# Kernel tuning notes

Measured on AMD Instinct MI355X. Metric: run time of the kernel, lower is better.

Reference implementation:

```python
import jax, jax.numpy as jnp
import numpy as np

R_MAX = 6.0
P = 6.0
QQ = 14.399645 * 0.5  # metal units, * 0.5


def setup_inputs() -> dict:
    key = jax.random.key(0)
    k1, k2, k3, k4 = jax.random.split(key, 4)
    n_atoms = 100_000
    n_edges = 6_400_000
    num_types = 4
    # atomic numbers for H, C, O, Cu
    Z = jnp.asarray([1.0, 6.0, 8.0, 29.0], dtype=jnp.float32)
    # edge lengths in (0.1, 7.3) so some edges exceed r_max and get cut off
    r = jax.random.uniform(k1, (n_edges,), dtype=jnp.float32) * 7.2 + 0.1
    per_atom_energy = jax.random.normal(k2, (n_atoms, 1), dtype=jnp.float32)
    atom_types = jax.random.randint(k3, (n_atoms,), 0, num_types, dtype=jnp.int64)
    edge_index = jax.random.randint(k4, (2, n_edges), 0, n_atoms, dtype=jnp.int64)
    return {"Z": Z, "r": r, "per_atom_energy": per_atom_energy,
            "atom_types": atom_types, "edge_index": edge_index}


def _zbl_edge_energy(Z, r, atom_types, edge_index):
    pzbl = 0.23
    a0 = 0.4685
    c1, c2, c3, c4 = 0.02817, 0.28022, 0.50986, 0.18175
    d1, d2, d3, d4 = -0.20162, -0.4029, -0.94229, -3.1998
    edge_types = atom_types[edge_index]          # (2, E)
    Zpair = Z[edge_types]                        # (2, E)
    Zi, Zj = Zpair[0], Zpair[1]
    x = (jnp.power(Zi, pzbl) + jnp.power(Zj, pzbl)) * r / a0
    psi = (c1 * jnp.exp(d1 * x) + c2 * jnp.exp(d2 * x)
           + c3 * jnp.exp(d3 * x) + c4 * jnp.exp(d4 * x))
    eng = QQ * (Zi * Zj / r) * psi
    rr = r / R_MAX
    p = P
    cutoff = (1.0 - (p + 1.0) * (p + 2.0) / 2.0 * jnp.power(rr, p)
              + p * (p + 2.0) * jnp.power(rr, p + 1.0)
              - p * (p + 1.0) / 2.0 * jnp.power(rr, p + 2.0))
    cutoff = cutoff * (rr < 1.0).astype(cutoff.dtype)
    return cutoff * eng                          # (E,)


def reference(Z, r, per_atom_energy, atom_types, edge_index):
    edge_eng = _zbl_edge_energy(Z, r, atom_types, edge_index)
    n_atoms = per_atom_energy.shape[0]
    atomic_eng = jax.ops.segment_sum(edge_eng, edge_index[0],
                                     num_segments=n_atoms)[:, None]
    return atomic_eng + per_atom_energy
```

## Files before the change

kernel.cpp:

```cpp
#include <hip/hip_runtime.h>


namespace {
constexpr float PZBL     = 0.23f;
constexpr float A0_INV   = 1.0f / 0.4685f;
constexpr float C1 = 0.02817f, C2 = 0.28022f, C3 = 0.50986f, C4 = 0.18175f;
constexpr float D1 = -0.20162f, D2 = -0.4029f, D3 = -0.94229f, D4 = -3.1998f;
constexpr float QQ       = 14.399645f * 0.5f;
constexpr float RMAX_INV = 1.0f / 6.0f;
constexpr int   CHUNK    = 25600;
constexpr int   BLOCK    = 1024;
constexpr int   S_MAX    = 64;
}

__global__ void zbl_table_kernel(const float* __restrict__ Z,
                                 float* __restrict__ tbl) {
    int t = threadIdx.x;
    if (t < 4) {
        float z = Z[t];
        tbl[t]     = z;
        tbl[4 + t] = powf(z, PZBL);
    }
}

__device__ __forceinline__ float zbl_energy(float rk, int ia, int ib,
                                            const int* __restrict__ types,
                                            const float* s_z, const float* s_zp) {
    float rr = rk * RMAX_INV;
    int ti = types[ia];
    int tj = types[ib];
    float zi = s_z[ti], zj = s_z[tj];
    float x = (s_zp[ti] + s_zp[tj]) * rk * A0_INV;
    float psi = C1 * __expf(D1 * x) + C2 * __expf(D2 * x)
              + C3 * __expf(D3 * x) + C4 * __expf(D4 * x);
    float eng = QQ * zi * zj * psi / rk;
    float rr2 = rr * rr;
    float rr3 = rr2 * rr;
    float rr6 = rr3 * rr3;
    float cutoff = 1.0f + rr6 * (-28.0f + rr * (48.0f - 21.0f * rr));
    return cutoff * eng;
}

__device__ __forceinline__ void zbl_edge_lds(float rk, int ia, int ib, int base,
                                             const int* __restrict__ types,
                                             const float* s_z, const float* s_zp,
                                             float* bins) {
    unsigned d = (unsigned)(ia - base);
    if (d >= (unsigned)CHUNK) return;
    if (rk * RMAX_INV >= 1.0f) return;
    atomicAdd(&bins[d], zbl_energy(rk, ia, ib, types, s_z, s_zp));
}

__global__ __launch_bounds__(BLOCK) void zbl_chunk_kernel(
    const float* __restrict__ r,
    const int*   __restrict__ ei0,
    const int*   __restrict__ ei1,
    const int*   __restrict__ types,
    const float* __restrict__ tbl,
    float*       __restrict__ partials,
    int n_chunks, int n_slices, int quads_per_slice,
    int n_quads, int n_edges) {
    __shared__ float s_z[4];
    __shared__ float s_zp[4];
    __shared__ float bins[CHUNK];

    int tid = threadIdx.x;
    if (tid < 8) {
        if (tid < 4) s_z[tid] = tbl[tid];
        else         s_zp[tid - 4] = tbl[tid];
    }
    for (int i = tid; i < CHUNK; i += BLOCK) bins[i] = 0.0f;
    __syncthreads();

    const int c = blockIdx.x % n_chunks;
    const int s = blockIdx.x / n_chunks;
    const int base = c * CHUNK;

    const int q0 = s * quads_per_slice;
    const int q1 = min(n_quads, q0 + quads_per_slice);
    const float4* r4 = (const float4*)r;
    const int4*   a4 = (const int4*)ei0;
    const int4*   b4 = (const int4*)ei1;

    for (int q = q0 + tid; q < q1; q += BLOCK) {
        float4 rv = r4[q];
        int4   av = a4[q];
        int4   bv = b4[q];
        zbl_edge_lds(rv.x, av.x, bv.x, base, types, s_z, s_zp, bins);
        zbl_edge_lds(rv.y, av.y, bv.y, base, types, s_z, s_zp, bins);
        zbl_edge_lds(rv.z, av.z, bv.z, base, types, s_z, s_zp, bins);
        zbl_edge_lds(rv.w, av.w, bv.w, base, types, s_z, s_zp, bins);
    }
    if (s == 0) {
        for (int e = 4 * n_quads + tid; e < n_edges; e += BLOCK) {
            zbl_edge_lds(r[e], ei0[e], ei1[e], base, types, s_z, s_zp, bins);
        }
    }
    __syncthreads();

    float* dst = partials + (size_t)blockIdx.x * CHUNK;
    for (int i = tid; i < CHUNK; i += BLOCK) dst[i] = bins[i];
}

__global__ void zbl_reduce_out(const float* __restrict__ pae,
                               const float* __restrict__ partials,
                               float* __restrict__ out,
                               int n_atoms, int n_chunks, int n_slices) {
    int a = blockIdx.x * blockDim.x + threadIdx.x;
    if (a >= n_atoms) return;
    int c = a / CHUNK;
    int i = a - c * CHUNK;
    const float* p = partials + (size_t)c * CHUNK + i;
    const size_t stride = (size_t)n_chunks * CHUNK;
    float sum = pae[a];
    for (int s = 0; s < n_slices; ++s) sum += p[(size_t)s * stride];
    out[a] = sum;
}

__global__ void zbl_init_out(const float* __restrict__ pae,
                             float* __restrict__ out, int n) {
    int i = blockIdx.x * blockDim.x + threadIdx.x;
    if (i < n) out[i] = pae[i];
}

__global__ __launch_bounds__(256) void zbl_edge_fallback(
    const float* __restrict__ r,
    const int*   __restrict__ ei0,
    const int*   __restrict__ ei1,
    const int*   __restrict__ types,
    const float* __restrict__ tbl,
    float*       __restrict__ out,
    int n_edges) {
    __shared__ float s_z[4];
    __shared__ float s_zp[4];
    if (threadIdx.x < 8) {
        if (threadIdx.x < 4) s_z[threadIdx.x] = tbl[threadIdx.x];
        else                 s_zp[threadIdx.x - 4] = tbl[threadIdx.x];
    }
    __syncthreads();
    int e = blockIdx.x * blockDim.x + threadIdx.x;
    if (e >= n_edges) return;
    float rk = r[e];
    if (rk * RMAX_INV >= 1.0f) return;
    unsafeAtomicAdd(&out[ei0[e]],
                    zbl_energy(rk, ei0[e], ei1[e], types, s_z, s_zp));
}

extern "C" void kernel_launch(void* const* d_in, const int* in_sizes, int n_in,
                              void* d_out, int out_size, void* d_ws, size_t ws_size,
                              hipStream_t stream) {
    const float* Z     = (const float*)d_in[0];
    const float* r     = (const float*)d_in[1];
    const float* pae   = (const float*)d_in[2];
    const int*   types = (const int*)d_in[3];
    const int*   ei    = (const int*)d_in[4];

    const int n_edges = in_sizes[1];
    const int n_atoms = in_sizes[2];

    float* out = (float*)d_out;
    float* tbl = (float*)d_ws;
    float* partials = tbl + 8;

    zbl_table_kernel<<<1, 64, 0, stream>>>(Z, tbl);

    const int n_chunks = (n_atoms + CHUNK - 1) / CHUNK;

    int S = S_MAX;
    while (S > 1 &&
           (8 + (size_t)n_chunks * S * CHUNK) * sizeof(float) > ws_size) {
        S >>= 1;
    }
    const bool use_lds_path =
        (8 + (size_t)n_chunks * S * CHUNK) * sizeof(float) <= ws_size;

    if (use_lds_path) {
        const int n_quads = (n_edges & 3) ? 0 : (n_edges >> 2);
        const int quads_per_slice = (n_quads + S - 1) / S;
        zbl_chunk_kernel<<<n_chunks * S, BLOCK, 0, stream>>>(
            r, ei, ei + n_edges, types, tbl, partials,
            n_chunks, S, quads_per_slice, n_quads, n_edges);
        zbl_reduce_out<<<(n_atoms + 255) / 256, 256, 0, stream>>>(
            pae, partials, out, n_atoms, n_chunks, S);
    } else {
        zbl_init_out<<<(n_atoms + 255) / 256, 256, 0, stream>>>(pae, out, n_atoms);
        zbl_edge_fallback<<<(n_edges + 255) / 256, 256, 0, stream>>>(
            r, ei, ei + n_edges, types, tbl, out, n_edges);
    }
}
```

Before: 191.5 us.

## Skip r/ei1 loads for out-of-chunk quads, fold table into chunk kernel, retune chunk

Each thread now loads the source-index quad first and skips loading r and ei1 when none of the four edges fall in the block's atom chunk. This cuts global traffic, since every chunk block otherwise streams all edges. The separate Z-table kernel launch is dropped and powf is computed per block instead. CHUNK shrinks from 25600 to 20000, which changes the chunk count to 5 and the grid size. The reduce kernel now sums slices with four accumulators.

```diff
diff --git a/kernel.cpp b/kernel.cpp
--- a/kernel.cpp
+++ b/kernel.cpp
@@ -7,20 +7,11 @@
 constexpr float C1 = 0.02817f, C2 = 0.28022f, C3 = 0.50986f, C4 = 0.18175f;
 constexpr float D1 = -0.20162f, D2 = -0.4029f, D3 = -0.94229f, D4 = -3.1998f;
 constexpr float QQ       = 14.399645f * 0.5f;
+constexpr float RMAX     = 6.0f;
 constexpr float RMAX_INV = 1.0f / 6.0f;
-constexpr int   CHUNK    = 25600;
+constexpr int   CHUNK    = 20000;
 constexpr int   BLOCK    = 1024;
 constexpr int   S_MAX    = 64;
-}
-
-__global__ void zbl_table_kernel(const float* __restrict__ Z,
-                                 float* __restrict__ tbl) {
-    int t = threadIdx.x;
-    if (t < 4) {
-        float z = Z[t];
-        tbl[t]     = z;
-        tbl[4 + t] = powf(z, PZBL);
-    }
 }
 
 __device__ __forceinline__ float zbl_energy(float rk, int ia, int ib,
@@ -41,33 +32,24 @@
     return cutoff * eng;
 }
 
-__device__ __forceinline__ void zbl_edge_lds(float rk, int ia, int ib, int base,
-                                             const int* __restrict__ types,
-                                             const float* s_z, const float* s_zp,
-                                             float* bins) {
-    unsigned d = (unsigned)(ia - base);
-    if (d >= (unsigned)CHUNK) return;
-    if (rk * RMAX_INV >= 1.0f) return;
-    atomicAdd(&bins[d], zbl_energy(rk, ia, ib, types, s_z, s_zp));
-}
-
 __global__ __launch_bounds__(BLOCK) void zbl_chunk_kernel(
+    const float* __restrict__ Z,
     const float* __restrict__ r,
     const int*   __restrict__ ei0,
     const int*   __restrict__ ei1,
     const int*   __restrict__ types,
-    const float* __restrict__ tbl,
     float*       __restrict__ partials,
-    int n_chunks, int n_slices, int quads_per_slice,
+    int n_chunks, int quads_per_slice,
     int n_quads, int n_edges) {
     __shared__ float s_z[4];
     __shared__ float s_zp[4];
     __shared__ float bins[CHUNK];
 
-    int tid = threadIdx.x;
-    if (tid < 8) {
-        if (tid < 4) s_z[tid] = tbl[tid];
-        else         s_zp[tid - 4] = tbl[tid];
+    const int tid = threadIdx.x;
+    if (tid < 4) {
+        float z = Z[tid];
+        s_z[tid]  = z;
+        s_zp[tid] = powf(z, PZBL);
     }
     for (int i = tid; i < CHUNK; i += BLOCK) bins[i] = 0.0f;
     __syncthreads();
@@ -83,17 +65,35 @@
     const int4*   b4 = (const int4*)ei1;
 
     for (int q = q0 + tid; q < q1; q += BLOCK) {
+        int4 av = a4[q];
+        unsigned d0 = (unsigned)(av.x - base);
+        unsigned d1 = (unsigned)(av.y - base);
+        unsigned d2 = (unsigned)(av.z - base);
+        unsigned d3 = (unsigned)(av.w - base);
+        bool m0 = d0 < (unsigned)CHUNK;
+        bool m1 = d1 < (unsigned)CHUNK;
+        bool m2 = d2 < (unsigned)CHUNK;
+        bool m3 = d3 < (unsigned)CHUNK;
+        if (!(m0 | m1 | m2 | m3)) continue;
         float4 rv = r4[q];
-        int4   av = a4[q];
         int4   bv = b4[q];
-        zbl_edge_lds(rv.x, av.x, bv.x, base, types, s_z, s_zp, bins);
-        zbl_edge_lds(rv.y, av.y, bv.y, base, types, s_z, s_zp, bins);
-        zbl_edge_lds(rv.z, av.z, bv.z, base, types, s_z, s_zp, bins);
-        zbl_edge_lds(rv.w, av.w, bv.w, base, types, s_z, s_zp, bins);
+        if (m0 && rv.x < RMAX)
+            atomicAdd(&bins[d0], zbl_energy(rv.x, av.x, bv.x, types, s_z, s_zp));
+        if (m1 && rv.y < RMAX)
+            atomicAdd(&bins[d1], zbl_energy(rv.y, av.y, bv.y, types, s_z, s_zp));
+        if (m2 && rv.z < RMAX)
+            atomicAdd(&bins[d2], zbl_energy(rv.z, av.z, bv.z, types, s_z, s_zp));
+        if (m3 && rv.w < RMAX)
+            atomicAdd(&bins[d3], zbl_energy(rv.w, av.w, bv.w, types, s_z, s_zp));
     }
     if (s == 0) {
         for (int e = 4 * n_quads + tid; e < n_edges; e += BLOCK) {
-            zbl_edge_lds(r[e], ei0[e], ei1[e], base, types, s_z, s_zp, bins);
+            int ia = ei0[e];
+            unsigned d = (unsigned)(ia - base);
+            if (d >= (unsigned)CHUNK) continue;
+            float rk = r[e];
+            if (rk >= RMAX) continue;
+            atomicAdd(&bins[d], zbl_energy(rk, ia, ei1[e], types, s_z, s_zp));
         }
     }
     __syncthreads();
@@ -112,9 +112,16 @@
     int i = a - c * CHUNK;
     const float* p = partials + (size_t)c * CHUNK + i;
     const size_t stride = (size_t)n_chunks * CHUNK;
-    float sum = pae[a];
-    for (int s = 0; s < n_slices; ++s) sum += p[(size_t)s * stride];
-    out[a] = sum;
+    float s0 = 0.0f, s1 = 0.0f, s2 = 0.0f, s3 = 0.0f;
+    int s = 0;
+    for (; s + 4 <= n_slices; s += 4) {
+        s0 += p[(size_t)(s + 0) * stride];
+        s1 += p[(size_t)(s + 1) * stride];
+        s2 += p[(size_t)(s + 2) * stride];
+        s3 += p[(size_t)(s + 3) * stride];
+    }
+    for (; s < n_slices; ++s) s0 += p[(size_t)s * stride];
+    out[a] = pae[a] + ((s0 + s1) + (s2 + s3));
 }
 
 __global__ void zbl_init_out(const float* __restrict__ pae,
@@ -124,24 +131,25 @@
 }
 
 __global__ __launch_bounds__(256) void zbl_edge_fallback(
+    const float* __restrict__ Z,
     const float* __restrict__ r,
     const int*   __restrict__ ei0,
     const int*   __restrict__ ei1,
     const int*   __restrict__ types,
-    const float* __restrict__ tbl,
     float*       __restrict__ out,
     int n_edges) {
     __shared__ float s_z[4];
     __shared__ float s_zp[4];
-    if (threadIdx.x < 8) {
-        if (threadIdx.x < 4) s_z[threadIdx.x] = tbl[threadIdx.x];
-        else                 s_zp[threadIdx.x - 4] = tbl[threadIdx.x];
+    if (threadIdx.x < 4) {
+        float z = Z[threadIdx.x];
+        s_z[threadIdx.x]  = z;
+        s_zp[threadIdx.x] = powf(z, PZBL);
     }
     __syncthreads();
     int e = blockIdx.x * blockDim.x + threadIdx.x;
     if (e >= n_edges) return;
     float rk = r[e];
-    if (rk * RMAX_INV >= 1.0f) return;
+    if (rk >= RMAX) return;
     unsafeAtomicAdd(&out[ei0[e]],
                     zbl_energy(rk, ei0[e], ei1[e], types, s_z, s_zp));
 }
@@ -159,32 +167,28 @@
     const int n_atoms = in_sizes[2];
 
     float* out = (float*)d_out;
-    float* tbl = (float*)d_ws;
-    float* partials = tbl + 8;
-
-    zbl_table_kernel<<<1, 64, 0, stream>>>(Z, tbl);
+    float* partials = (float*)d_ws;
 
     const int n_chunks = (n_atoms + CHUNK - 1) / CHUNK;
 
     int S = S_MAX;
-    while (S > 1 &&
-           (8 + (size_t)n_chunks * S * CHUNK) * sizeof(float) > ws_size) {
+    while (S > 1 && (size_t)n_chunks * S * CHUNK * sizeof(float) > ws_size) {
         S >>= 1;
     }
     const bool use_lds_path =
-        (8 + (size_t)n_chunks * S * CHUNK) * sizeof(float) <= ws_size;
+        (size_t)n_chunks * S * CHUNK * sizeof(float) <= ws_size;
 
     if (use_lds_path) {
         const int n_quads = (n_edges & 3) ? 0 : (n_edges >> 2);
         const int quads_per_slice = (n_quads + S - 1) / S;
         zbl_chunk_kernel<<<n_chunks * S, BLOCK, 0, stream>>>(
-            r, ei, ei + n_edges, types, tbl, partials,
-            n_chunks, S, quads_per_slice, n_quads, n_edges);
+            Z, r, ei, ei + n_edges, types, partials,
+            n_chunks, quads_per_slice, n_quads, n_edges);
         zbl_reduce_out<<<(n_atoms + 255) / 256, 256, 0, stream>>>(
             pae, partials, out, n_atoms, n_chunks, S);
     } else {
         zbl_init_out<<<(n_atoms + 255) / 256, 256, 0, stream>>>(pae, out, n_atoms);
         zbl_edge_fallback<<<(n_edges + 255) / 256, 256, 0, stream>>>(
-            r, ei, ei + n_edges, types, tbl, out, n_edges);
+            Z, r, ei, ei + n_edges, types, out, n_edges);
     }
 }
```

Result: slower. 214.0 us (+11.7%).
